# Kernel optimization log

Measured on AMD Instinct MI355X. Metric: run time of the kernel, lower is better.

Reference implementation:

```python
import jax, jax.numpy as jnp
import numpy as np

ATLAS_DHW = (91, 109, 91)   # AAL atlas grid (MNI space)
ROI_LO, ROI_HI = 1, 94      # roi_range: labels 1..94 kept, 0 = background
NUM_SEG = ROI_HI + 1        # 95 segments (incl. background slot 0)


def setup_inputs() -> dict:
    key = jax.random.key(0)
    k1, k2 = jax.random.split(key)
    B, C = 2, 64
    feat = jax.random.normal(k1, (B, C, 96, 112, 96), dtype=jnp.float32)
    atlas = jax.random.randint(k2, ATLAS_DHW, 0, NUM_SEG, dtype=jnp.int32)
    return {"feat": feat, "atlas": atlas}


def reference(feat, atlas):
    # Crop padded feature map back to atlas grid
    D, H, W = ATLAS_DHW
    feat = feat[..., :D, :H, :W]                      # (B, C, D, H, W)
    B, C = feat.shape[0], feat.shape[1]
    N = D * H * W

    ids = atlas.reshape(-1)                           # (N,) voxel -> ROI label
    # (B, C, N) -> (N, B*C) so segment_sum reduces over voxels
    flat = jnp.moveaxis(feat.reshape(B, C, N), 2, 0).reshape(N, B * C)

    # Masked segment sum == one-hot matmul num = einsum('rn,bcn->brc')
    sums = jax.ops.segment_sum(flat, ids, num_segments=NUM_SEG)   # (95, B*C)
    cnts = jax.ops.segment_sum(jnp.ones((N,), feat.dtype), ids,
                               num_segments=NUM_SEG)              # (95,)

    num = sums[ROI_LO:].reshape(NUM_SEG - ROI_LO, B, C)           # (R, B, C)
    den = jnp.maximum(cnts[ROI_LO:], 1e-6)                        # (R,)
    out = jnp.transpose(num, (1, 0, 2)) / den[None, :, None]      # (B, R, C)
    return out
```

## Files before the change

### kernel.cpp

```cpp
#include <hip/hip_runtime.h>

constexpr int SEG_N   = 95;
constexpr int CROP_D  = 91, CROP_H = 109, CROP_W = 91;
constexpr int LINES   = CROP_D * CROP_H;
constexpr int FEAT_W  = 96;
constexpr int FEAT_HW = 112 * 96;
constexpr int CSTRIDE = 96 * 112 * 96;
constexpr int NTILE   = LINES * 3;
constexpr int PSEG    = 96;
constexpr int ROWS    = 129;
constexpr int BIN_SZ  = ROWS * PSEG;
constexpr int GRID    = 1024;
constexpr int NCHUNK  = 16;
constexpr int KPC     = GRID / NCHUNK;
constexpr int OUT_N   = 2 * 94 * 64;
constexpr size_t PART2_OFF = (size_t)GRID * BIN_SZ * sizeof(float);
constexpr size_t WS_NEED   = PART2_OFF + (size_t)NCHUNK * BIN_SZ * sizeof(float);

typedef __attribute__((ext_vector_type(8))) short bf16x8;
typedef __attribute__((ext_vector_type(4))) float f32x4;

__device__ inline unsigned int rne2(float a, float b) {
    unsigned int x = __float_as_uint(a), y = __float_as_uint(b);
    x = (x + 0x7FFFu + ((x >> 16) & 1u)) >> 16;
    y = (y + 0x7FFFu + ((y >> 16) & 1u)) & 0xFFFF0000u;
    return x | y;
}

__global__ __launch_bounds__(256) void zero_part(float* __restrict__ p)
{
    const int i = blockIdx.x * 256 + threadIdx.x;
    if (i < BIN_SZ) p[i] = 0.0f;
}

__global__ __launch_bounds__(256, 4) void seg_mfma(const float* __restrict__ feat,
                                                   const int*   __restrict__ atlas,
                                                   float* __restrict__ part,
                                                   int use_atomic)
{
    const int tid = threadIdx.x, wv = tid >> 6, lane = tid & 63;
    const int l15 = lane & 15, lq = lane >> 4;

    f32x4 acc[2][6];
    f32x4 accc[6];
    #pragma unroll
    for (int s = 0; s < 6; ++s) {
        acc[0][s] = (f32x4){0.f, 0.f, 0.f, 0.f};
        acc[1][s] = (f32x4){0.f, 0.f, 0.f, 0.f};
        accc[s]   = (f32x4){0.f, 0.f, 0.f, 0.f};
    }
    union { bf16x8 v; unsigned int u[4]; } ONES;
    ONES.u[0] = ONES.u[1] = ONES.u[2] = ONES.u[3] = 0x3F803F80u;

    const int base = NTILE / GRID, rem = NTILE % GRID;
    const int bx   = blockIdx.x;
    const int t0   = bx * base + (bx < rem ? bx : rem);
    const int te   = t0 + base + (bx < rem ? 1 : 0);

    for (int t = t0; t < te; ++t) {
        const int line  = t / 3;
        const int w0    = (t - line * 3) * 32;
        const int d     = line / CROP_H, h = line - d * CROP_H;
        const int lbase = d * FEAT_HW + h * FEAT_W + w0;

        int id[8];
        const int wq = w0 + lq * 8, abase = line * CROP_W + w0 + lq * 8;
        #pragma unroll
        for (int j = 0; j < 8; ++j)
            id[j] = (wq + j < CROP_W) ? atlas[abase + j] : 95;

        bf16x8 bv[6];
        #pragma unroll
        for (int sb = 0; sb < 6; ++sb) {
            const int seg = sb * 16 + l15;
            union { bf16x8 v; unsigned int u[4]; } B;
            #pragma unroll
            for (int p = 0; p < 4; ++p) {
                const unsigned int lo = (id[2 * p]     == seg) ? 0x3F80u     : 0u;
                const unsigned int hi = (id[2 * p + 1] == seg) ? 0x3F800000u : 0u;
                B.u[p] = lo | hi;
            }
            bv[sb] = B.v;
        }

        if (wv == 0) {
            #pragma unroll
            for (int sb = 0; sb < 6; ++sb)
                accc[sb] = __builtin_amdgcn_mfma_f32_16x16x32_bf16(ONES.v, bv[sb], accc[sb], 0, 0, 0);
        }

        #pragma unroll
        for (int a = 0; a < 2; ++a) {
            const int ch = wv * 32 + a * 16 + l15;
            const float* fp = feat + (size_t)ch * CSTRIDE + lbase + lq * 8;
            const float4 v0 = *(const float4*)fp;
            const float4 v1 = *(const float4*)(fp + 4);
            union { bf16x8 v; unsigned int u[4]; } A;
            A.u[0] = rne2(v0.x, v0.y); A.u[1] = rne2(v0.z, v0.w);
            A.u[2] = rne2(v1.x, v1.y); A.u[3] = rne2(v1.z, v1.w);
            #pragma unroll
            for (int sb = 0; sb < 6; ++sb)
                acc[a][sb] = __builtin_amdgcn_mfma_f32_16x16x32_bf16(A.v, bv[sb], acc[a][sb], 0, 0, 0);
        }
    }

    float* p = part + (use_atomic ? 0 : (size_t)blockIdx.x * BIN_SZ);
    #pragma unroll
    for (int a = 0; a < 2; ++a)
        #pragma unroll
        for (int sb = 0; sb < 6; ++sb)
            #pragma unroll
            for (int r = 0; r < 4; ++r) {
                const int i = (wv * 32 + a * 16 + lq * 4 + r) * PSEG + sb * 16 + l15;
                if (use_atomic) unsafeAtomicAdd(&p[i], acc[a][sb][r]);
                else            p[i] = acc[a][sb][r];
            }
    if (wv == 0 && lq == 0) {
        #pragma unroll
        for (int sb = 0; sb < 6; ++sb) {
            const int i = 128 * PSEG + sb * 16 + l15;
            if (use_atomic) unsafeAtomicAdd(&p[i], accc[sb][0]);
            else            p[i] = accc[sb][0];
        }
    }
}

__global__ __launch_bounds__(256) void reduce_stageA(const float* __restrict__ part,
                                                     float* __restrict__ part2)
{
    const int g = blockIdx.x * 256 + threadIdx.x;
    const int c = g / BIN_SZ, e = g - c * BIN_SZ;
    const float* p = part + (size_t)c * KPC * BIN_SZ + e;
    float s = 0.0f;
    #pragma unroll 8
    for (int k = 0; k < KPC; ++k) s += p[(size_t)k * BIN_SZ];
    part2[g] = s;
}

__global__ __launch_bounds__(256) void finalize(const float* __restrict__ src,
                                                float* __restrict__ out,
                                                int n)
{
    const int idx = blockIdx.x * 256 + threadIdx.x;
    if (idx >= OUT_N) return;
    const int c   = idx & 63;
    const int s0  = (idx >> 6) % 94;
    const int b   = idx / (94 * 64);
    const int seg = s0 + 1;
    const int ch  = b * 64 + c;
    float s = 0.0f, cnt = 0.0f;
    for (int k = 0; k < n; ++k) {
        s   += src[(size_t)k * BIN_SZ + ch * PSEG + seg];
        cnt += src[(size_t)k * BIN_SZ + 128 * PSEG + seg];
    }
    out[idx] = s / fmaxf(cnt, 1e-6f);
}

extern "C" void kernel_launch(void* const* d_in, const int* in_sizes, int n_in,
                              void* d_out, int out_size, void* d_ws, size_t ws_size,
                              hipStream_t stream)
{
    const float* feat  = (const float*)d_in[0];
    const int*   atlas = (const int*)d_in[1];
    float* out   = (float*)d_out;
    float* part  = (float*)d_ws;
    float* part2 = (float*)((char*)d_ws + PART2_OFF);
    const int use_atomic = (ws_size < WS_NEED) ? 1 : 0;

    if (use_atomic)
        zero_part<<<(BIN_SZ + 255) / 256, 256, 0, stream>>>(part);
    seg_mfma<<<GRID, 256, 0, stream>>>(feat, atlas, part, use_atomic);
    if (!use_atomic)
        reduce_stageA<<<(BIN_SZ * NCHUNK) / 256, 256, 0, stream>>>(part, part2);
    finalize<<<(OUT_N + 255) / 256, 256, 0, stream>>>(use_atomic ? part : part2, out,
                                                      use_atomic ? 1 : NCHUNK);
}
```

Measured before the change: 135.4 us.

## Stage feature super-tiles through LDS with coalesced row loads

```diff
diff --git a/kernel.cpp b/kernel.cpp
--- a/kernel.cpp
+++ b/kernel.cpp
@@ -1,12 +1,9 @@
 #include <hip/hip_runtime.h>
 
-constexpr int SEG_N   = 95;
 constexpr int CROP_D  = 91, CROP_H = 109, CROP_W = 91;
-constexpr int LINES   = CROP_D * CROP_H;
 constexpr int FEAT_W  = 96;
 constexpr int FEAT_HW = 112 * 96;
 constexpr int CSTRIDE = 96 * 112 * 96;
-constexpr int NTILE   = LINES * 3;
 constexpr int PSEG    = 96;
 constexpr int ROWS    = 129;
 constexpr int BIN_SZ  = ROWS * PSEG;
@@ -14,6 +11,9 @@
 constexpr int NCHUNK  = 16;
 constexpr int KPC     = GRID / NCHUNK;
 constexpr int OUT_N   = 2 * 94 * 64;
+constexpr int SPP     = 82;
+constexpr int NST     = CROP_D * SPP;
+constexpr int ROWB    = 288;
 constexpr size_t PART2_OFF = (size_t)GRID * BIN_SZ * sizeof(float);
 constexpr size_t WS_NEED   = PART2_OFF + (size_t)NCHUNK * BIN_SZ * sizeof(float);
 
@@ -38,8 +38,11 @@
                                                    float* __restrict__ part,
                                                    int use_atomic)
 {
+    __shared__ __align__(16) char lds[4 * 32 * ROWB];
     const int tid = threadIdx.x, wv = tid >> 6, lane = tid & 63;
     const int l15 = lane & 15, lq = lane >> 4;
+    const int l5  = lane & 31, c2 = lane >> 5;
+    char* slice = lds + wv * 32 * ROWB;
 
     f32x4 acc[2][6];
     f32x4 accc[6];
@@ -52,55 +55,67 @@
     union { bf16x8 v; unsigned int u[4]; } ONES;
     ONES.u[0] = ONES.u[1] = ONES.u[2] = ONES.u[3] = 0x3F803F80u;
 
-    const int base = NTILE / GRID, rem = NTILE % GRID;
+    const int base = NST / GRID, rem = NST % GRID;
     const int bx   = blockIdx.x;
-    const int t0   = bx * base + (bx < rem ? bx : rem);
-    const int te   = t0 + base + (bx < rem ? 1 : 0);
+    const int st0  = bx * base + (bx < rem ? bx : rem);
+    const int st1  = st0 + base + (bx < rem ? 1 : 0);
 
-    for (int t = t0; t < te; ++t) {
-        const int line  = t / 3;
-        const int w0    = (t - line * 3) * 32;
-        const int d     = line / CROP_H, h = line - d * CROP_H;
-        const int lbase = d * FEAT_HW + h * FEAT_W + w0;
+    for (int st = st0; st < st1; ++st) {
+        const int d  = st / SPP, s = st - d * SPP;
+        const int nt = (s < SPP - 1) ? 4 : 3;
 
-        int id[8];
-        const int wq = w0 + lq * 8, abase = line * CROP_W + w0 + lq * 8;
+        const float* fb = feat + (size_t)(wv * 32) * CSTRIDE + d * FEAT_HW + s * 128 + l5 * 4;
         #pragma unroll
-        for (int j = 0; j < 8; ++j)
-            id[j] = (wq + j < CROP_W) ? atlas[abase + j] : 95;
-
-        bf16x8 bv[6];
-        #pragma unroll
-        for (int sb = 0; sb < 6; ++sb) {
-            const int seg = sb * 16 + l15;
-            union { bf16x8 v; unsigned int u[4]; } B;
+        for (int g = 0; g < 4; ++g) {
+            float4 pay[4];
             #pragma unroll
-            for (int p = 0; p < 4; ++p) {
-                const unsigned int lo = (id[2 * p]     == seg) ? 0x3F80u     : 0u;
-                const unsigned int hi = (id[2 * p + 1] == seg) ? 0x3F800000u : 0u;
-                B.u[p] = lo | hi;
+            for (int i = 0; i < 4; ++i)
+                pay[i] = *(const float4*)(fb + (size_t)(g * 8 + i * 2 + c2) * CSTRIDE);
+            #pragma unroll
+            for (int i = 0; i < 4; ++i) {
+                const int chl = g * 8 + i * 2 + c2;
+                uint2 w; w.x = rne2(pay[i].x, pay[i].y); w.y = rne2(pay[i].z, pay[i].w);
+                *(uint2*)(slice + chl * ROWB + l5 * 8) = w;
             }
-            bv[sb] = B.v;
         }
 
-        if (wv == 0) {
+        for (int ts = 0; ts < nt; ++ts) {
+            const int tp = s * 4 + ts;
+            const int h  = tp / 3, w0 = (tp - h * 3) * 32;
+            const int wq = w0 + lq * 8;
+            const int ab = (d * CROP_H + h) * CROP_W + wq;
+            int id[8];
             #pragma unroll
-            for (int sb = 0; sb < 6; ++sb)
-                accc[sb] = __builtin_amdgcn_mfma_f32_16x16x32_bf16(ONES.v, bv[sb], accc[sb], 0, 0, 0);
-        }
+            for (int j = 0; j < 8; ++j)
+                id[j] = (wq + j < CROP_W) ? atlas[ab + j] : 95;
 
-        #pragma unroll
-        for (int a = 0; a < 2; ++a) {
-            const int ch = wv * 32 + a * 16 + l15;
-            const float* fp = feat + (size_t)ch * CSTRIDE + lbase + lq * 8;
-            const float4 v0 = *(const float4*)fp;
-            const float4 v1 = *(const float4*)(fp + 4);
-            union { bf16x8 v; unsigned int u[4]; } A;
-            A.u[0] = rne2(v0.x, v0.y); A.u[1] = rne2(v0.z, v0.w);
-            A.u[2] = rne2(v1.x, v1.y); A.u[3] = rne2(v1.z, v1.w);
+            bf16x8 bv[6];
             #pragma unroll
-            for (int sb = 0; sb < 6; ++sb)
-                acc[a][sb] = __builtin_amdgcn_mfma_f32_16x16x32_bf16(A.v, bv[sb], acc[a][sb], 0, 0, 0);
+            for (int sb = 0; sb < 6; ++sb) {
+                const int seg = sb * 16 + l15;
+                union { bf16x8 v; unsigned int u[4]; } B;
+                #pragma unroll
+                for (int p = 0; p < 4; ++p) {
+                    const unsigned int lo = (id[2 * p]     == seg) ? 0x3F80u     : 0u;
+                    const unsigned int hi = (id[2 * p + 1] == seg) ? 0x3F800000u : 0u;
+                    B.u[p] = lo | hi;
+                }
+                bv[sb] = B.v;
+            }
+
+            if (wv == 0) {
+                #pragma unroll
+                for (int sb = 0; sb < 6; ++sb)
+                    accc[sb] = __builtin_amdgcn_mfma_f32_16x16x32_bf16(ONES.v, bv[sb], accc[sb], 0, 0, 0);
+            }
+
+            #pragma unroll
+            for (int a = 0; a < 2; ++a) {
+                const bf16x8 av = *(const bf16x8*)(slice + (a * 16 + l15) * ROWB + ts * 64 + lq * 16);
+                #pragma unroll
+                for (int sb = 0; sb < 6; ++sb)
+                    acc[a][sb] = __builtin_amdgcn_mfma_f32_16x16x32_bf16(av, bv[sb], acc[a][sb], 0, 0, 0);
+            }
         }
     }
 
```

New measurement: 177.6 us. 1.31x slower.

## Double-buffer tile loads in MFMA loop and move voxel counts to separate kernel

Applied to the files above, without the earlier changes.

```diff
diff --git a/kernel.cpp b/kernel.cpp
--- a/kernel.cpp
+++ b/kernel.cpp
@@ -1,21 +1,22 @@
 #include <hip/hip_runtime.h>
 
-constexpr int SEG_N   = 95;
 constexpr int CROP_D  = 91, CROP_H = 109, CROP_W = 91;
+constexpr int NVOX    = CROP_D * CROP_H * CROP_W;
 constexpr int LINES   = CROP_D * CROP_H;
 constexpr int FEAT_W  = 96;
 constexpr int FEAT_HW = 112 * 96;
 constexpr int CSTRIDE = 96 * 112 * 96;
 constexpr int NTILE   = LINES * 3;
 constexpr int PSEG    = 96;
-constexpr int ROWS    = 129;
-constexpr int BIN_SZ  = ROWS * PSEG;
+constexpr int BIN_SZ  = 128 * PSEG;
 constexpr int GRID    = 1024;
 constexpr int NCHUNK  = 16;
 constexpr int KPC     = GRID / NCHUNK;
+constexpr int NCB     = 64;
 constexpr int OUT_N   = 2 * 94 * 64;
-constexpr size_t PART2_OFF = (size_t)GRID * BIN_SZ * sizeof(float);
-constexpr size_t WS_NEED   = PART2_OFF + (size_t)NCHUNK * BIN_SZ * sizeof(float);
+constexpr size_t P2_OFF  = (size_t)GRID * BIN_SZ * sizeof(float);
+constexpr size_t CNT_OFF = P2_OFF + (size_t)NCHUNK * BIN_SZ * sizeof(float);
+constexpr size_t WS_NEED = CNT_OFF + (size_t)NCB * PSEG * sizeof(int);
 
 typedef __attribute__((ext_vector_type(8))) short bf16x8;
 typedef __attribute__((ext_vector_type(4))) float f32x4;
@@ -25,6 +26,51 @@
     x = (x + 0x7FFFu + ((x >> 16) & 1u)) >> 16;
     y = (y + 0x7FFFu + ((y >> 16) & 1u)) & 0xFFFF0000u;
     return x | y;
+}
+
+struct TileBuf {
+    float4 p00, p01, p10, p11;
+    int id[8];
+};
+
+__device__ inline void load_tile(const float* __restrict__ fb0,
+                                 const float* __restrict__ fb1,
+                                 const int*   __restrict__ atlas,
+                                 int t, int lq, TileBuf& b)
+{
+    const int line = t / 3, w0 = (t - line * 3) * 32;
+    const int d = line / CROP_H, h = line - d * CROP_H;
+    const int lb = d * FEAT_HW + h * FEAT_W + w0 + lq * 8;
+    b.p00 = *(const float4*)(fb0 + lb);
+    b.p01 = *(const float4*)(fb0 + lb + 4);
+    b.p10 = *(const float4*)(fb1 + lb);
+    b.p11 = *(const float4*)(fb1 + lb + 4);
+    const int wq = w0 + lq * 8, ab = line * CROP_W + wq;
+    #pragma unroll
+    for (int j = 0; j < 8; ++j)
+        b.id[j] = (wq + j < CROP_W) ? atlas[ab + j] : 95;
+}
+
+__device__ inline void compute_tile(const TileBuf& b, int l15, f32x4 acc[2][6])
+{
+    union { bf16x8 v; unsigned int u[4]; } A0, A1;
+    A0.u[0] = rne2(b.p00.x, b.p00.y); A0.u[1] = rne2(b.p00.z, b.p00.w);
+    A0.u[2] = rne2(b.p01.x, b.p01.y); A0.u[3] = rne2(b.p01.z, b.p01.w);
+    A1.u[0] = rne2(b.p10.x, b.p10.y); A1.u[1] = rne2(b.p10.z, b.p10.w);
+    A1.u[2] = rne2(b.p11.x, b.p11.y); A1.u[3] = rne2(b.p11.z, b.p11.w);
+    #pragma unroll
+    for (int sb = 0; sb < 6; ++sb) {
+        const int seg = sb * 16 + l15;
+        union { bf16x8 v; unsigned int u[4]; } B;
+        #pragma unroll
+        for (int p = 0; p < 4; ++p) {
+            const unsigned int lo = (b.id[2 * p]     == seg) ? 0x3F80u     : 0u;
+            const unsigned int hi = (b.id[2 * p + 1] == seg) ? 0x3F800000u : 0u;
+            B.u[p] = lo | hi;
+        }
+        acc[0][sb] = __builtin_amdgcn_mfma_f32_16x16x32_bf16(A0.v, B.v, acc[0][sb], 0, 0, 0);
+        acc[1][sb] = __builtin_amdgcn_mfma_f32_16x16x32_bf16(A1.v, B.v, acc[1][sb], 0, 0, 0);
+    }
 }
 
 __global__ __launch_bounds__(256) void zero_part(float* __restrict__ p)
@@ -42,69 +88,34 @@
     const int l15 = lane & 15, lq = lane >> 4;
 
     f32x4 acc[2][6];
-    f32x4 accc[6];
     #pragma unroll
     for (int s = 0; s < 6; ++s) {
         acc[0][s] = (f32x4){0.f, 0.f, 0.f, 0.f};
         acc[1][s] = (f32x4){0.f, 0.f, 0.f, 0.f};
-        accc[s]   = (f32x4){0.f, 0.f, 0.f, 0.f};
     }
-    union { bf16x8 v; unsigned int u[4]; } ONES;
-    ONES.u[0] = ONES.u[1] = ONES.u[2] = ONES.u[3] = 0x3F803F80u;
 
     const int base = NTILE / GRID, rem = NTILE % GRID;
     const int bx   = blockIdx.x;
     const int t0   = bx * base + (bx < rem ? bx : rem);
-    const int te   = t0 + base + (bx < rem ? 1 : 0);
+    const int t1   = t0 + base + (bx < rem ? 1 : 0);
 
-    for (int t = t0; t < te; ++t) {
-        const int line  = t / 3;
-        const int w0    = (t - line * 3) * 32;
-        const int d     = line / CROP_H, h = line - d * CROP_H;
-        const int lbase = d * FEAT_HW + h * FEAT_W + w0;
+    const float* fb0 = feat + (size_t)(wv * 32 + l15) * CSTRIDE;
+    const float* fb1 = feat + (size_t)(wv * 32 + 16 + l15) * CSTRIDE;
 
-        int id[8];
-        const int wq = w0 + lq * 8, abase = line * CROP_W + w0 + lq * 8;
-        #pragma unroll
-        for (int j = 0; j < 8; ++j)
-            id[j] = (wq + j < CROP_W) ? atlas[abase + j] : 95;
-
-        bf16x8 bv[6];
-        #pragma unroll
-        for (int sb = 0; sb < 6; ++sb) {
-            const int seg = sb * 16 + l15;
-            union { bf16x8 v; unsigned int u[4]; } B;
-            #pragma unroll
-            for (int p = 0; p < 4; ++p) {
-                const unsigned int lo = (id[2 * p]     == seg) ? 0x3F80u     : 0u;
-                const unsigned int hi = (id[2 * p + 1] == seg) ? 0x3F800000u : 0u;
-                B.u[p] = lo | hi;
-            }
-            bv[sb] = B.v;
-        }
-
-        if (wv == 0) {
-            #pragma unroll
-            for (int sb = 0; sb < 6; ++sb)
-                accc[sb] = __builtin_amdgcn_mfma_f32_16x16x32_bf16(ONES.v, bv[sb], accc[sb], 0, 0, 0);
-        }
-
-        #pragma unroll
-        for (int a = 0; a < 2; ++a) {
-            const int ch = wv * 32 + a * 16 + l15;
-            const float* fp = feat + (size_t)ch * CSTRIDE + lbase + lq * 8;
-            const float4 v0 = *(const float4*)fp;
-            const float4 v1 = *(const float4*)(fp + 4);
-            union { bf16x8 v; unsigned int u[4]; } A;
-            A.u[0] = rne2(v0.x, v0.y); A.u[1] = rne2(v0.z, v0.w);
-            A.u[2] = rne2(v1.x, v1.y); A.u[3] = rne2(v1.z, v1.w);
-            #pragma unroll
-            for (int sb = 0; sb < 6; ++sb)
-                acc[a][sb] = __builtin_amdgcn_mfma_f32_16x16x32_bf16(A.v, bv[sb], acc[a][sb], 0, 0, 0);
-        }
+    TileBuf bufA, bufB;
+    load_tile(fb0, fb1, atlas, t0, lq, bufA);
+    int t = t0;
+    while (t < t1) {
+        if (t + 1 < t1) load_tile(fb0, fb1, atlas, t + 1, lq, bufB);
+        compute_tile(bufA, l15, acc);
+        ++t;
+        if (t >= t1) break;
+        if (t + 1 < t1) load_tile(fb0, fb1, atlas, t + 1, lq, bufA);
+        compute_tile(bufB, l15, acc);
+        ++t;
     }
 
-    float* p = part + (use_atomic ? 0 : (size_t)blockIdx.x * BIN_SZ);
+    float* p = part + (use_atomic ? 0 : (size_t)bx * BIN_SZ);
     #pragma unroll
     for (int a = 0; a < 2; ++a)
         #pragma unroll
@@ -115,14 +126,19 @@
                 if (use_atomic) unsafeAtomicAdd(&p[i], acc[a][sb][r]);
                 else            p[i] = acc[a][sb][r];
             }
-    if (wv == 0 && lq == 0) {
-        #pragma unroll
-        for (int sb = 0; sb < 6; ++sb) {
-            const int i = 128 * PSEG + sb * 16 + l15;
-            if (use_atomic) unsafeAtomicAdd(&p[i], accc[sb][0]);
-            else            p[i] = accc[sb][0];
-        }
-    }
+}
+
+__global__ __launch_bounds__(256) void seg_count(const int* __restrict__ atlas,
+                                                 int* __restrict__ cslot)
+{
+    __shared__ int cbin[PSEG];
+    const int tid = threadIdx.x;
+    if (tid < PSEG) cbin[tid] = 0;
+    __syncthreads();
+    for (int i = blockIdx.x * 256 + tid; i < NVOX; i += NCB * 256)
+        atomicAdd(&cbin[atlas[i]], 1);
+    __syncthreads();
+    if (tid < PSEG) cslot[blockIdx.x * PSEG + tid] = cbin[tid];
 }
 
 __global__ __launch_bounds__(256) void reduce_stageA(const float* __restrict__ part,
@@ -138,6 +154,7 @@
 }
 
 __global__ __launch_bounds__(256) void finalize(const float* __restrict__ src,
+                                                const int*   __restrict__ cslot,
                                                 float* __restrict__ out,
                                                 int n)
 {
@@ -148,12 +165,13 @@
     const int b   = idx / (94 * 64);
     const int seg = s0 + 1;
     const int ch  = b * 64 + c;
-    float s = 0.0f, cnt = 0.0f;
-    for (int k = 0; k < n; ++k) {
-        s   += src[(size_t)k * BIN_SZ + ch * PSEG + seg];
-        cnt += src[(size_t)k * BIN_SZ + 128 * PSEG + seg];
-    }
-    out[idx] = s / fmaxf(cnt, 1e-6f);
+    float s = 0.0f;
+    for (int k = 0; k < n; ++k)
+        s += src[(size_t)k * BIN_SZ + ch * PSEG + seg];
+    int cnt = 0;
+    #pragma unroll 8
+    for (int k = 0; k < NCB; ++k) cnt += cslot[k * PSEG + seg];
+    out[idx] = s / fmaxf((float)cnt, 1e-6f);
 }
 
 extern "C" void kernel_launch(void* const* d_in, const int* in_sizes, int n_in,
@@ -162,16 +180,19 @@
 {
     const float* feat  = (const float*)d_in[0];
     const int*   atlas = (const int*)d_in[1];
-    float* out   = (float*)d_out;
-    float* part  = (float*)d_ws;
-    float* part2 = (float*)((char*)d_ws + PART2_OFF);
+    float* out  = (float*)d_out;
+    float* part = (float*)d_ws;
     const int use_atomic = (ws_size < WS_NEED) ? 1 : 0;
+    float* part2 = use_atomic ? part : (float*)((char*)d_ws + P2_OFF);
+    int*   cslot = use_atomic ? (int*)((char*)d_ws + (size_t)BIN_SZ * sizeof(float))
+                              : (int*)((char*)d_ws + CNT_OFF);
 
     if (use_atomic)
         zero_part<<<(BIN_SZ + 255) / 256, 256, 0, stream>>>(part);
+    seg_count<<<NCB, 256, 0, stream>>>(atlas, cslot);
     seg_mfma<<<GRID, 256, 0, stream>>>(feat, atlas, part, use_atomic);
     if (!use_atomic)
         reduce_stageA<<<(BIN_SZ * NCHUNK) / 256, 256, 0, stream>>>(part, part2);
-    finalize<<<(OUT_N + 255) / 256, 256, 0, stream>>>(use_atomic ? part : part2, out,
+    finalize<<<(OUT_N + 255) / 256, 256, 0, stream>>>(part2, cslot, out,
                                                       use_atomic ? 1 : NCHUNK);
 }
```

Result: slower. 334.4 us (+146.9%).
